# Performance work log

Measured on AMD Instinct MI355X. Metric: run time of the kernel, lower is better.

## Reference

```python
import jax, jax.numpy as jnp
import numpy as np

B = 512
NODES_PER_GRAPH = 256
N = B * NODES_PER_GRAPH
IN_DIM = 128
HID = 128
PAD_VALUE = -10000.0


def setup_inputs() -> dict:
    key = jax.random.key(0)
    ks = jax.random.split(key, 10)
    inp = {
        "last_node_batch": jax.random.normal(ks[0], (B, IN_DIM), jnp.float32),
        "h": jax.random.normal(ks[1], (N, HID), jnp.float32),
        # NodeEmbed: Linear(in_dim, hidden_dim)
        "W_embed": jax.random.normal(ks[2], (IN_DIM, HID), jnp.float32) / np.sqrt(IN_DIM),
        "b_embed": jnp.zeros((HID,), jnp.float32),
        # Linear_3(2H, 2H, 2)
        "W1": jax.random.normal(ks[3], (2 * HID, 2 * HID), jnp.float32) / np.sqrt(2 * HID),
        "b1": jnp.zeros((2 * HID,), jnp.float32),
        "W2": jax.random.normal(ks[4], (2 * HID, 2 * HID), jnp.float32) / np.sqrt(2 * HID),
        "b2": jnp.zeros((2 * HID,), jnp.float32),
        "W3": jax.random.normal(ks[5], (2 * HID, 2), jnp.float32) / np.sqrt(2 * HID),
        "b3": jnp.zeros((2,), jnp.float32),
        # ragged batch encoded as sorted segment ids (graph id per node)
        "segment_ids": jnp.repeat(jnp.arange(B, dtype=jnp.int64), NODES_PER_GRAPH),
        "max_nodes": NODES_PER_GRAPH,
    }
    return inp


def reference(last_node_batch, h, W_embed, b_embed, W1, b1, W2, b2, W3, b3,
              segment_ids, max_nodes):
    n = h.shape[0]
    b = last_node_batch.shape[0]
    # per-graph node embed, broadcast to each node of its graph (repeat+cat loop)
    node_embed = last_node_batch @ W_embed + b_embed          # [B, H]
    bcast = node_embed[segment_ids]                           # [N, H]
    stack = jnp.concatenate([h, bcast], axis=1)               # [N, 2H]
    # Linear_3 MLP
    out = jnp.tanh(stack @ W1 + b1)
    out = jnp.tanh(out @ W2 + b2)
    edges = out @ W3 + b3                                     # [N, 2]
    # unbatch + pad_sequence(padding_value=-10000), then flatten(1, -1)
    counts = jax.ops.segment_sum(jnp.ones((n,), jnp.int32), segment_ids, num_segments=b)
    offsets = jnp.cumsum(counts) - counts                     # start index of each graph
    pos = jnp.arange(n) - offsets[segment_ids]                # position within graph
    padded = jnp.full((b, max_nodes, 2), PAD_VALUE, dtype=edges.dtype)
    padded = padded.at[segment_ids, pos].set(edges)
    return padded.reshape(b, max_nodes * 2)
```

## Files before the change

### kernel.cpp

```cpp
#include <hip/hip_runtime.h>


typedef __attribute__((ext_vector_type(8))) short s16x8;
typedef __attribute__((ext_vector_type(4))) float f32x4;

#define K2   256
#define KH   128
#define LDK  264

__device__ __forceinline__ float b2f(unsigned short u) {
  return __builtin_bit_cast(float, (unsigned int)u << 16);
}
__device__ __forceinline__ unsigned short f2b(float f) {
  unsigned int u = __builtin_bit_cast(unsigned int, f);
  u += 0x7fffu + ((u >> 16) & 1u);
  return (unsigned short)(u >> 16);
}
__device__ __forceinline__ unsigned int pk2(float a, float b) {
  return (unsigned int)f2b(a) | ((unsigned int)f2b(b) << 16);
}
__device__ __forceinline__ float pade_tanh(float x) {
  float x2 = x * x;
  float x4 = x2 * x2;
  float num = x * (945.0f + 105.0f * x2 + x4);
  float den = __builtin_fmaf(15.0f, x4, __builtin_fmaf(420.0f, x2, 945.0f));
  float r = num * __builtin_amdgcn_rcpf(den);
  return __builtin_fmaxf(-1.0f, __builtin_fminf(1.0f, r));
}
__device__ __forceinline__ unsigned int probe_is16(const unsigned int* wraw,
                                                   int t) {
  unsigned int w = wraw[t];
  unsigned int e = (w >> 7) & 0xFFu;
  unsigned long long m = __ballot(e >= 96 && e < 128);
  return (__popcll(m) >= 32) ? 1u : 0u;
}

__global__ __launch_bounds__(256) void prep_pack(
    const void* __restrict__ W1, const void* __restrict__ W2,
    const void* __restrict__ Wemb,
    unsigned short* __restrict__ W1P, unsigned short* __restrict__ W2P,
    unsigned short* __restrict__ W1loP)
{
  __shared__ unsigned int flagLds;
  const int blk = blockIdx.x, t = threadIdx.x;
  if (t < 64) { unsigned int f = probe_is16((const unsigned int*)Wemb, t);
                if (t == 0) flagLds = f; }
  __syncthreads();
  const bool is16 = flagLds != 0u;

  const void* S; unsigned short* D; int k0, n0, pk, krow;
  if (blk < 32) { S = W1; D = W1P; pk = 2048; krow = 0;
                  k0 = (blk & 3) * 32; n0 = (blk >> 2) * 32; }
  else if (blk < 96) { int b = blk - 32; S = W2; D = W2P; pk = 4096; krow = 0;
                       k0 = (b & 7) * 32; n0 = (b >> 3) * 32; }
  else { int b = blk - 96; S = W1; D = W1loP; pk = 2048; krow = KH;
         k0 = (b & 3) * 32; n0 = (b >> 2) * 32; }
  #pragma unroll
  for (int q = 0; q < 4; ++q) {
    int idx = t + 256 * q;
    int ln = idx & 31, lk = idx >> 5;
    int n = n0 + ln, k = k0 + lk;
    unsigned short v = is16
        ? ((const unsigned short*)S)[(krow + k) * K2 + n]
        : f2b(((const float*)S)[(krow + k) * K2 + n]);
    D[(n >> 4) * pk + (k >> 3) * 128 + (n & 15) * 8 + (k & 7)] = v;
  }
}

__global__ __launch_bounds__(256, 2) void mlp_graph(
    const void* __restrict__ h,     const void* __restrict__ last,
    const void* __restrict__ Wemb,  const void* __restrict__ bemb,
    const void* __restrict__ b1,    const void* __restrict__ b2,
    const void* __restrict__ W3,    const void* __restrict__ b3,
    const unsigned short* __restrict__ W1P,
    const unsigned short* __restrict__ W2P,
    const unsigned short* __restrict__ W1loP,
    void* __restrict__ out)
{
  __shared__ __align__(16) unsigned short smA[64 * LDK];
  __shared__ float embp[2][KH];
  __shared__ __align__(16) unsigned short embb[KH];
  __shared__ __align__(16) unsigned short w3lds[3][K2];
  __shared__ __align__(16) float ebias[K2];
  __shared__ __align__(16) float b2s[K2];
  __shared__ unsigned int flagLds;

  const int t    = threadIdx.x;
  const int lane = t & 63, w = t >> 6;
  const int quad = lane >> 4, l16 = lane & 15;
  const int gb   = blockIdx.x;
  const int g    = gb >> 1;
  const int row0 = g * 256 + (gb & 1) * 128;

  if (t < 64) { unsigned int f = probe_is16((const unsigned int*)Wemb, t);
                if (t == 0) flagLds = f; }
  __syncthreads();
  const bool is16 = flagLds != 0u;

  uint4 hreg[4];
  const int pr = t >> 4, pc = t & 15;
  auto load_tile = [&](int tile) {
    int rbase = row0 + tile * 64;
    if (is16) {
      const uint4* hp = (const uint4*)h;
      #pragma unroll
      for (int i = 0; i < 4; ++i)
        hreg[i] = hp[(size_t)(rbase + pr + 16 * i) * 16 + pc];
    } else {
      const float4* hf = (const float4*)h;
      #pragma unroll
      for (int i = 0; i < 4; ++i) {
        float4 va = hf[(size_t)(rbase + pr + 16 * i) * 32 + pc * 2];
        float4 vb = hf[(size_t)(rbase + pr + 16 * i) * 32 + pc * 2 + 1];
        hreg[i] = make_uint4(pk2(va.x, va.y), pk2(va.z, va.w),
                             pk2(vb.x, vb.y), pk2(vb.z, vb.w));
      }
    }
  };
  load_tile(0);

  {
    const int j = t & 127, kh2 = t >> 7, k0 = kh2 * 64;
    float a0 = 0.f, a1 = 0.f, a2 = 0.f, a3 = 0.f;
    if (is16) {
      const unsigned short* lp = (const unsigned short*)last + g * KH;
      const unsigned short* wp = (const unsigned short*)Wemb;
      #pragma unroll 4
      for (int k = k0; k < k0 + 64; k += 4) {
        a0 += b2f(lp[k])     * b2f(wp[k * KH + j]);
        a1 += b2f(lp[k + 1]) * b2f(wp[(k + 1) * KH + j]);
        a2 += b2f(lp[k + 2]) * b2f(wp[(k + 2) * KH + j]);
        a3 += b2f(lp[k + 3]) * b2f(wp[(k + 3) * KH + j]);
      }
    } else {
      const float* lp = (const float*)last + g * KH;
      const float* wp = (const float*)Wemb;
      #pragma unroll 4
      for (int k = k0; k < k0 + 64; k += 4) {
        a0 += lp[k]     * wp[k * KH + j];
        a1 += lp[k + 1] * wp[(k + 1) * KH + j];
        a2 += lp[k + 2] * wp[(k + 2) * KH + j];
        a3 += lp[k + 3] * wp[(k + 3) * KH + j];
      }
    }
    embp[kh2][j] = (a0 + a1) + (a2 + a3);
  }
  for (int s = t; s < 2 * K2; s += 256) {
    int e = s & 1, k = s >> 1;
    w3lds[e][k] = is16 ? ((const unsigned short*)W3)[k * 2 + e]
                       : f2b(((const float*)W3)[k * 2 + e]);
  }
  w3lds[2][t] = 0;
  b2s[t] = is16 ? b2f(((const unsigned short*)b2)[t]) : ((const float*)b2)[t];
  float b30 = is16 ? b2f(((const unsigned short*)b3)[0]) : ((const float*)b3)[0];
  float b31 = is16 ? b2f(((const unsigned short*)b3)[1]) : ((const float*)b3)[1];
  __syncthreads();

  if (t < KH) {
    float e = is16 ? b2f(((const unsigned short*)bemb)[t])
                   : ((const float*)bemb)[t];
    embb[t] = f2b(e + embp[0][t] + embp[1][t]);
  }
  __syncthreads();

  {
    f32x4 eacc[4];
    #pragma unroll
    for (int i = 0; i < 4; ++i) eacc[i] = f32x4{0.f, 0.f, 0.f, 0.f};
    #pragma unroll
    for (int kk = 0; kk < 4; ++kk) {
      s16x8 be = *(const s16x8*)&embb[kk * 32 + quad * 8];
      #pragma unroll
      for (int i = 0; i < 4; ++i) {
        s16x8 a = *(const s16x8*)&W1loP[(w * 4 + i) * 2048
                                        + (kk * 4 + quad) * 128 + l16 * 8];
        eacc[i] = __builtin_amdgcn_mfma_f32_16x16x32_bf16(a, be, eacc[i],
                                                          0, 0, 0);
      }
    }
    if (l16 == 0) {
      #pragma unroll
      for (int i = 0; i < 4; ++i)
        #pragma unroll
        for (int rg = 0; rg < 4; ++rg) {
          int f = (w * 4 + i) * 16 + quad * 4 + rg;
          float bb = is16 ? b2f(((const unsigned short*)b1)[f])
                          : ((const float*)b1)[f];
          ebias[f] = bb + eacc[i][rg];
        }
    }
  }

  f32x4 acc[4][4];
  for (int tile = 0; tile < 2; ++tile) {
    const int base = row0 + tile * 64;
    __syncthreads();
    #pragma unroll
    for (int i = 0; i < 4; ++i)
      *(uint4*)&smA[(pr + 16 * i) * LDK + pc * 8] = hreg[i];
    if (tile == 0) load_tile(1);
    __syncthreads();

    #pragma unroll
    for (int i = 0; i < 4; ++i) {
      f32x4 e = *(const f32x4*)&ebias[(w * 4 + i) * 16 + quad * 4];
      #pragma unroll
      for (int c = 0; c < 4; ++c) acc[i][c] = e;
    }
    #pragma unroll
    for (int kk = 0; kk < 4; ++kk) {
      s16x8 bf[4];
      #pragma unroll
      for (int c = 0; c < 4; ++c)
        bf[c] = *(const s16x8*)&smA[(c * 16 + l16) * LDK + kk * 32 + quad * 8];
      #pragma unroll
      for (int i = 0; i < 4; ++i) {
        s16x8 a = *(const s16x8*)&W1P[(w * 4 + i) * 2048
                                      + (kk * 4 + quad) * 128 + l16 * 8];
        #pragma unroll
        for (int c = 0; c < 4; ++c)
          acc[i][c] = __builtin_amdgcn_mfma_f32_16x16x32_bf16(
              a, bf[c], acc[i][c], 0, 0, 0);
      }
    }
    __syncthreads();
    #pragma unroll
    for (int i = 0; i < 4; ++i)
      #pragma unroll
      for (int c = 0; c < 4; ++c) {
        uint2 d;
        d.x = pk2(pade_tanh(acc[i][c][0]), pade_tanh(acc[i][c][1]));
        d.y = pk2(pade_tanh(acc[i][c][2]), pade_tanh(acc[i][c][3]));
        *(uint2*)&smA[(c * 16 + l16) * LDK + (w * 4 + i) * 16 + quad * 4] = d;
      }
    __syncthreads();

    #pragma unroll
    for (int i = 0; i < 4; ++i) {
      f32x4 e = *(const f32x4*)&b2s[(w * 4 + i) * 16 + quad * 4];
      #pragma unroll
      for (int c = 0; c < 4; ++c) acc[i][c] = e;
    }
    #pragma unroll 2
    for (int kk = 0; kk < 8; ++kk) {
      s16x8 bf[4];
      #pragma unroll
      for (int c = 0; c < 4; ++c)
        bf[c] = *(const s16x8*)&smA[(c * 16 + l16) * LDK + kk * 32 + quad * 8];
      #pragma unroll
      for (int i = 0; i < 4; ++i) {
        s16x8 a = *(const s16x8*)&W2P[(w * 4 + i) * 4096
                                      + (kk * 4 + quad) * 128 + l16 * 8];
        #pragma unroll
        for (int c = 0; c < 4; ++c)
          acc[i][c] = __builtin_amdgcn_mfma_f32_16x16x32_bf16(
              a, bf[c], acc[i][c], 0, 0, 0);
      }
    }
    __syncthreads();
    #pragma unroll
    for (int i = 0; i < 4; ++i)
      #pragma unroll
      for (int c = 0; c < 4; ++c) {
        uint2 d;
        d.x = pk2(pade_tanh(acc[i][c][0]), pade_tanh(acc[i][c][1]));
        d.y = pk2(pade_tanh(acc[i][c][2]), pade_tanh(acc[i][c][3]));
        *(uint2*)&smA[(c * 16 + l16) * LDK + (w * 4 + i) * 16 + quad * 4] = d;
      }
    __syncthreads();

    {
      f32x4 hacc = f32x4{0.f, 0.f, 0.f, 0.f};
      const unsigned short* w3row = w3lds[l16 < 2 ? l16 : 2];
      #pragma unroll
      for (int kk = 0; kk < 8; ++kk) {
        s16x8 a3 = *(const s16x8*)&w3row[kk * 32 + quad * 8];
        s16x8 bf = *(const s16x8*)&smA[(w * 16 + l16) * LDK
                                       + kk * 32 + quad * 8];
        hacc = __builtin_amdgcn_mfma_f32_16x16x32_bf16(a3, bf, hacc, 0, 0, 0);
      }
      if (quad == 0) {
        int node = base + w * 16 + l16;
        float e0 = hacc[0] + b30, e1 = hacc[1] + b31;
        if (is16) ((unsigned int*)out)[node] = pk2(e0, e1);
        else *(float2*)((float*)out + (size_t)node * 2) = make_float2(e0, e1);
      }
    }
  }
}

extern "C" void kernel_launch(void* const* d_in, const int* in_sizes, int n_in,
                              void* d_out, int out_size, void* d_ws, size_t ws_size,
                              hipStream_t stream) {
  (void)in_sizes; (void)n_in; (void)out_size; (void)ws_size;
  const void* last = d_in[0];
  const void* h    = d_in[1];
  const void* Wemb = d_in[2];
  const void* bemb = d_in[3];
  const void* W1   = d_in[4];
  const void* b1   = d_in[5];
  const void* W2   = d_in[6];
  const void* b2   = d_in[7];
  const void* W3   = d_in[8];
  const void* b3   = d_in[9];

  char* ws = (char*)d_ws;
  unsigned short* W1P   = (unsigned short*)(ws);
  unsigned short* W2P   = (unsigned short*)(ws + 65536);
  unsigned short* W1loP = (unsigned short*)(ws + 196608);

  prep_pack<<<dim3(128), dim3(256), 0, stream>>>(W1, W2, Wemb, W1P, W2P, W1loP);
  mlp_graph<<<dim3(1024), dim3(256), 0, stream>>>(
      h, last, Wemb, bemb, b1, b2, W3, b3, W1P, W2P, W1loP, d_out);
}
```

Baseline: 169.3 us.

## Process one graph per block with double-buffered h tiles and register-resident W1

Each block now handles a whole graph (4 tiles of 64 rows) instead of half a graph, so the per-graph embedding and W1-low bias work is done once rather than twice. The h input gets a separate double-buffered LDS region, so the next tile's global load and LDS store overlap with the current tile's layer-1 MFMAs, which removes a couple of barriers per tile. The W1 fragments are loaded into registers once and reused across tiles instead of being re-read from global memory each time. In exchange, register pressure and LDS use go up, and the grid is halved to 512 blocks, which may reduce occupancy and latency hiding on a GPU with many CUs.

```diff
diff --git a/kernel.cpp b/kernel.cpp
--- a/kernel.cpp
+++ b/kernel.cpp
@@ -6,7 +6,8 @@
 
 #define K2   256
 #define KH   128
-#define LDK  264
+#define LDH  136
+#define LDA  264
 
 __device__ __forceinline__ float b2f(unsigned short u) {
   return __builtin_bit_cast(float, (unsigned int)u << 16);
@@ -77,7 +78,8 @@
     const unsigned short* __restrict__ W1loP,
     void* __restrict__ out)
 {
-  __shared__ __align__(16) unsigned short smA[64 * LDK];
+  __shared__ __align__(16) unsigned short smH[2][64 * LDH];
+  __shared__ __align__(16) unsigned short smAct[64 * LDA];
   __shared__ float embp[2][KH];
   __shared__ __align__(16) unsigned short embb[KH];
   __shared__ __align__(16) unsigned short w3lds[3][K2];
@@ -88,18 +90,16 @@
   const int t    = threadIdx.x;
   const int lane = t & 63, w = t >> 6;
   const int quad = lane >> 4, l16 = lane & 15;
-  const int gb   = blockIdx.x;
-  const int g    = gb >> 1;
-  const int row0 = g * 256 + (gb & 1) * 128;
+  const int g    = blockIdx.x;
+  const int row0 = g * 256;
 
   if (t < 64) { unsigned int f = probe_is16((const unsigned int*)Wemb, t);
                 if (t == 0) flagLds = f; }
   __syncthreads();
   const bool is16 = flagLds != 0u;
 
-  uint4 hreg[4];
   const int pr = t >> 4, pc = t & 15;
-  auto load_tile = [&](int tile) {
+  auto load_tile = [&](int tile, uint4* hreg) {
     int rbase = row0 + tile * 64;
     if (is16) {
       const uint4* hp = (const uint4*)h;
@@ -117,7 +117,17 @@
       }
     }
   };
-  load_tile(0);
+  auto store_tile = [&](int buf, const uint4* hreg) {
+    #pragma unroll
+    for (int i = 0; i < 4; ++i)
+      *(uint4*)&smH[buf][(pr + 16 * i) * LDH + pc * 8] = hreg[i];
+  };
+
+  {
+    uint4 hreg[4];
+    load_tile(0, hreg);
+    store_tile(0, hreg);
+  }
 
   {
     const int j = t & 127, kh2 = t >> 7, k0 = kh2 * 64;
@@ -154,6 +164,14 @@
   b2s[t] = is16 ? b2f(((const unsigned short*)b2)[t]) : ((const float*)b2)[t];
   float b30 = is16 ? b2f(((const unsigned short*)b3)[0]) : ((const float*)b3)[0];
   float b31 = is16 ? b2f(((const unsigned short*)b3)[1]) : ((const float*)b3)[1];
+
+  s16x8 w1f[16];
+  #pragma unroll
+  for (int kk = 0; kk < 4; ++kk)
+    #pragma unroll
+    for (int i = 0; i < 4; ++i)
+      w1f[kk * 4 + i] = *(const s16x8*)&W1P[(w * 4 + i) * 2048
+                                            + (kk * 4 + quad) * 128 + l16 * 8];
   __syncthreads();
 
   if (t < KH) {
@@ -190,16 +208,15 @@
         }
     }
   }
+  __syncthreads();
 
   f32x4 acc[4][4];
-  for (int tile = 0; tile < 2; ++tile) {
+  for (int tile = 0; tile < 4; ++tile) {
+    const int buf  = tile & 1;
     const int base = row0 + tile * 64;
-    __syncthreads();
-    #pragma unroll
-    for (int i = 0; i < 4; ++i)
-      *(uint4*)&smA[(pr + 16 * i) * LDK + pc * 8] = hreg[i];
-    if (tile == 0) load_tile(1);
-    __syncthreads();
+
+    uint4 hreg[4];
+    if (tile < 3) load_tile(tile + 1, hreg);
 
     #pragma unroll
     for (int i = 0; i < 4; ++i) {
@@ -212,18 +229,16 @@
       s16x8 bf[4];
       #pragma unroll
       for (int c = 0; c < 4; ++c)
-        bf[c] = *(const s16x8*)&smA[(c * 16 + l16) * LDK + kk * 32 + quad * 8];
-      #pragma unroll
-      for (int i = 0; i < 4; ++i) {
-        s16x8 a = *(const s16x8*)&W1P[(w * 4 + i) * 2048
-                                      + (kk * 4 + quad) * 128 + l16 * 8];
+        bf[c] = *(const s16x8*)&smH[buf][(c * 16 + l16) * LDH
+                                         + kk * 32 + quad * 8];
+      #pragma unroll
+      for (int i = 0; i < 4; ++i)
         #pragma unroll
         for (int c = 0; c < 4; ++c)
           acc[i][c] = __builtin_amdgcn_mfma_f32_16x16x32_bf16(
-              a, bf[c], acc[i][c], 0, 0, 0);
-      }
-    }
-    __syncthreads();
+              w1f[kk * 4 + i], bf[c], acc[i][c], 0, 0, 0);
+    }
+    if (tile < 3) store_tile(buf ^ 1, hreg);
     #pragma unroll
     for (int i = 0; i < 4; ++i)
       #pragma unroll
@@ -231,7 +246,7 @@
         uint2 d;
         d.x = pk2(pade_tanh(acc[i][c][0]), pade_tanh(acc[i][c][1]));
         d.y = pk2(pade_tanh(acc[i][c][2]), pade_tanh(acc[i][c][3]));
-        *(uint2*)&smA[(c * 16 + l16) * LDK + (w * 4 + i) * 16 + quad * 4] = d;
+        *(uint2*)&smAct[(c * 16 + l16) * LDA + (w * 4 + i) * 16 + quad * 4] = d;
       }
     __syncthreads();
 
@@ -246,7 +261,8 @@
       s16x8 bf[4];
       #pragma unroll
       for (int c = 0; c < 4; ++c)
-        bf[c] = *(const s16x8*)&smA[(c * 16 + l16) * LDK + kk * 32 + quad * 8];
+        bf[c] = *(const s16x8*)&smAct[(c * 16 + l16) * LDA
+                                      + kk * 32 + quad * 8];
       #pragma unroll
       for (int i = 0; i < 4; ++i) {
         s16x8 a = *(const s16x8*)&W2P[(w * 4 + i) * 4096
@@ -265,7 +281,7 @@
         uint2 d;
         d.x = pk2(pade_tanh(acc[i][c][0]), pade_tanh(acc[i][c][1]));
         d.y = pk2(pade_tanh(acc[i][c][2]), pade_tanh(acc[i][c][3]));
-        *(uint2*)&smA[(c * 16 + l16) * LDK + (w * 4 + i) * 16 + quad * 4] = d;
+        *(uint2*)&smAct[(c * 16 + l16) * LDA + (w * 4 + i) * 16 + quad * 4] = d;
       }
     __syncthreads();
 
@@ -275,8 +291,8 @@
       #pragma unroll
       for (int kk = 0; kk < 8; ++kk) {
         s16x8 a3 = *(const s16x8*)&w3row[kk * 32 + quad * 8];
-        s16x8 bf = *(const s16x8*)&smA[(w * 16 + l16) * LDK
-                                       + kk * 32 + quad * 8];
+        s16x8 bf = *(const s16x8*)&smAct[(w * 16 + l16) * LDA
+                                         + kk * 32 + quad * 8];
         hacc = __builtin_amdgcn_mfma_f32_16x16x32_bf16(a3, bf, hacc, 0, 0, 0);
       }
       if (quad == 0) {
@@ -286,6 +302,7 @@
         else *(float2*)((float*)out + (size_t)node * 2) = make_float2(e0, e1);
       }
     }
+    __syncthreads();
   }
 }
 
@@ -310,6 +327,6 @@
   unsigned short* W1loP = (unsigned short*)(ws + 196608);
 
   prep_pack<<<dim3(128), dim3(256), 0, stream>>>(W1, W2, Wemb, W1P, W2P, W1loP);
-  mlp_graph<<<dim3(1024), dim3(256), 0, stream>>>(
+  mlp_graph<<<dim3(512), dim3(256), 0, stream>>>(
       h, last, Wemb, bemb, b1, b2, W3, b3, W1P, W2P, W1loP, d_out);
 }
```

Result: faster. 161.3 us (-4.7%).
